# Optimization experiments

Hardware: AMD Instinct MI355X
Metric: run time of the kernel (lower is better)

Reference implementation:

```python
import jax, jax.numpy as jnp
import numpy as np

B = 512          # batch == number of memories
S = 8            # num_attention_splits
U = 512          # num_units = sum(num_units_regions)
D = 32           # dim_attention_unit
G = 8            # num_attention_groups
MASK_P = 0.1
DIM_IN = 4096
DAG = 2048       # dim_attention_global


def setup_inputs() -> dict:
    key = jax.random.key(0)
    ks = jax.random.split(key, 8)
    # xavier-normal-ish scales for the unit-wise linears
    s1 = (2.0 / (DIM_IN // S + DAG // S)) ** 0.5
    s2 = (2.0 / (DAG // S + U * D // S)) ** 0.5
    return {
        "x": jax.random.normal(ks[0], (B, DIM_IN), jnp.float32),
        "mem_attention": jax.random.normal(ks[1], (B, U, D), jnp.float32),
        "mem_outputs": jax.random.normal(ks[2], (B, U, D), jnp.float32),
        "rand_u": jax.random.uniform(ks[3], (B, B, U), jnp.float32),
        "w1": jax.random.normal(ks[4], (S, DIM_IN // S, DAG // S), jnp.float32) * s1,
        "b1": jnp.zeros((S, DAG // S), jnp.float32),
        "w2": jax.random.normal(ks[5], (S, DAG // S, U * D // S), jnp.float32) * s2,
        "b2": jnp.zeros((S, U * D // S), jnp.float32),
        "temperature": jnp.ones((U,), jnp.float32),
    }


def reference(x, mem_attention, mem_outputs, rand_u, w1, b1, w2, b2, temperature):
    # attentions(): split input, two unit-wise linears
    xs = x.reshape(B, S, DIM_IN // S)                        # [B,S,I/S]
    ga = jnp.einsum("bsi,sio->bso", xs, w1) + b1             # [B,S,DAG/S]
    att = jnp.einsum("bso,soj->bsj", ga, w2) + b2            # [B,S,U*D/S]
    att = att.reshape(B, U, D)                               # [B,U,D]
    ga_flat = ga.reshape(B, DAG)                             # [B,DAG]

    # per-unit pairwise scores: (att_b . mem_att_m) per unit  -> [B,M,U]
    weights = jnp.einsum("bud,mud->bmu", att, mem_attention)
    weights = weights * temperature                          # broadcast over U

    neg_inf = jnp.float32(-jnp.inf)
    weights = jnp.where(rand_u < MASK_P, neg_inf, weights)   # random mask
    eye = jnp.eye(B, dtype=bool)[:, :, None]                 # self-exclusion
    weights = jnp.where(eye, neg_inf, weights)

    # group-wise softmax over the memory axis
    w = weights.reshape(B, B // G, G, U)
    w = jax.nn.softmax(w, axis=1)
    w = w.reshape(B, B, U) / 8.0

    # weighted reduction over memories (avoids [B,B,U,D] intermediate)
    outputs = jnp.einsum("bmu,mud->bud", w, mem_outputs)     # [B,U,D]
    return att, ga_flat, w, outputs
```

## Files before the change

kernel.cpp:

```cpp
#include <hip/hip_runtime.h>
#include <math.h>

#define NEGBIG (-1e30f)
#define GLB_PTR(x) ((const __attribute__((address_space(1))) void*)(x))
#define LDS_PTR(x) ((__attribute__((address_space(3))) void*)(x))

typedef __bf16 bf16x8 __attribute__((ext_vector_type(8)));
typedef float  f32x4  __attribute__((ext_vector_type(4)));


__global__ __launch_bounds__(256) void gemm_split(
    const float* __restrict__ A, int lda, int Ksz,
    const float* __restrict__ Bw, int NS,
    const float* __restrict__ bias,
    float* __restrict__ C, int ldc)
{
  const int n0 = blockIdx.x * 64;
  const int b0 = blockIdx.y * 64;
  const int s  = n0 / NS;
  const float* Bp = Bw + (size_t)s * Ksz * NS;
  const int nloc0 = n0 - s * NS;
  const int acol0 = s * Ksz;

  __shared__ float As[16][64];
  __shared__ float Bs[16][64];

  const int t  = threadIdx.x;
  const int tb = t & 15, tn = t >> 4;
  float acc[4][4] = {};

  for (int k0 = 0; k0 < Ksz; k0 += 16) {
    {
      int r = t & 63, g = t >> 6;
      float4 v = *reinterpret_cast<const float4*>(
          A + (size_t)(b0 + r) * lda + acol0 + k0 + 4 * g);
      As[4*g+0][r] = v.x; As[4*g+1][r] = v.y; As[4*g+2][r] = v.z; As[4*g+3][r] = v.w;
    }
    {
      int kk = t >> 4, n4 = t & 15;
      float4 v = *reinterpret_cast<const float4*>(
          Bp + (size_t)(k0 + kk) * NS + nloc0 + 4 * n4);
      *reinterpret_cast<float4*>(&Bs[kk][4*n4]) = v;
    }
    __syncthreads();
#pragma unroll
    for (int k = 0; k < 16; ++k) {
      float4 a4 = *reinterpret_cast<const float4*>(&As[k][4*tb]);
      float4 b4 = *reinterpret_cast<const float4*>(&Bs[k][4*tn]);
      float av[4] = {a4.x, a4.y, a4.z, a4.w};
      float bv[4] = {b4.x, b4.y, b4.z, b4.w};
#pragma unroll
      for (int i = 0; i < 4; ++i)
#pragma unroll
        for (int j = 0; j < 4; ++j)
          acc[i][j] = fmaf(av[i], bv[j], acc[i][j]);
    }
    __syncthreads();
  }
#pragma unroll
  for (int i = 0; i < 4; ++i) {
    int row = b0 + 4*tb + i;
    int col = n0 + 4*tn;
    float4 o;
    o.x = acc[i][0] + bias[col + 0];
    o.y = acc[i][1] + bias[col + 1];
    o.z = acc[i][2] + bias[col + 2];
    o.w = acc[i][3] + bias[col + 3];
    *reinterpret_cast<float4*>(C + (size_t)row * ldc + col) = o;
  }
}

__global__ __launch_bounds__(256) void scores_mfma_v5(
    const float* __restrict__ att,
    const float* __restrict__ ma,
    const float* __restrict__ rnd,
    const float* __restrict__ temp,
    float* __restrict__ wout,
    float* __restrict__ stats)
{
  __shared__ float MaL[2048 * 4];
  __shared__ float tr[256 * 17];
  const int b0 = blockIdx.x * 16;
  const int u0 = blockIdx.y * 16;
  const int t  = threadIdx.x;
  const int w  = t >> 6, l = t & 63;
  const int lm = l & 15, kb = l >> 4;
  const int eu = t & 15, eb = t >> 4;
  const int gbe = b0 + eb;

  const float tmp = temp[u0 + eu];

  bf16x8 Ahi[4], Alo[4];
#pragma unroll
  for (int q = 0; q < 4; ++q) {
    const float* ap = att + (size_t)(b0 + lm) * 16384
                    + (size_t)(u0 + 4 * w + q) * 32 + kb * 8;
    float4 a0 = *reinterpret_cast<const float4*>(ap);
    float4 a1 = *reinterpret_cast<const float4*>(ap + 4);
    float af[8] = {a0.x, a0.y, a0.z, a0.w, a1.x, a1.y, a1.z, a1.w};
#pragma unroll
    for (int j = 0; j < 8; ++j) {
      __bf16 h = (__bf16)af[j];
      Ahi[q][j] = h;
      Alo[q][j] = (__bf16)(af[j] - (float)h);
    }
  }

  int off[8];
#pragma unroll
  for (int k = 0; k < 8; ++k) {
    int s = k * 256 + t;
    int mm = s >> 7, uu = (s >> 3) & 15, d4s = s & 7;
    off[k] = mm * 16384 + (u0 + uu) * 32 + ((d4s ^ (mm & 7)) << 2);
  }

  float Ls[8];
#pragma unroll
  for (int g = 0; g < 8; ++g) Ls[g] = 0.f;

  const float* rbase = rnd  + (size_t)gbe * 262144 + u0 + eu;
  float*       wbase = wout + (size_t)gbe * 262144 + u0 + eu;

#pragma unroll
  for (int k = 0; k < 8; ++k)
    __builtin_amdgcn_global_load_lds(GLB_PTR(ma + (size_t)off[k]),
                                     LDS_PTR(&MaL[(k * 256 + w * 64) * 4]), 16, 0, 0);
  float rc[16], rn[16];
#pragma unroll
  for (int j = 0; j < 16; ++j) rc[j] = rbase[(size_t)j * 512];

#pragma unroll 1
  for (int c = 0; c < 32; ++c) {
    const int m0 = c * 16;
    __syncthreads();

#pragma unroll
    for (int q = 0; q < 4; ++q) {
      const int uq = 4 * w + q;
      const int s0 = (lm << 7) + (uq << 3) + ((2 * kb)     ^ (lm & 7));
      const int s1 = (lm << 7) + (uq << 3) + ((2 * kb + 1) ^ (lm & 7));
      float4 g0 = *reinterpret_cast<const float4*>(&MaL[s0 * 4]);
      float4 g1 = *reinterpret_cast<const float4*>(&MaL[s1 * 4]);
      float bf[8] = {g0.x, g0.y, g0.z, g0.w, g1.x, g1.y, g1.z, g1.w};
      bf16x8 Bhi, Blo;
#pragma unroll
      for (int j = 0; j < 8; ++j) {
        __bf16 h = (__bf16)bf[j];
        Bhi[j] = h;
        Blo[j] = (__bf16)(bf[j] - (float)h);
      }
      f32x4 a = {0.f, 0.f, 0.f, 0.f};
      a = __builtin_amdgcn_mfma_f32_16x16x32_bf16(Ahi[q], Blo, a, 0, 0, 0);
      a = __builtin_amdgcn_mfma_f32_16x16x32_bf16(Alo[q], Bhi, a, 0, 0, 0);
      a = __builtin_amdgcn_mfma_f32_16x16x32_bf16(Ahi[q], Bhi, a, 0, 0, 0);
#pragma unroll
      for (int i = 0; i < 4; ++i) {
        const int row = (kb * 4 + i) * 16 + lm;
        tr[row * 17 + (uq ^ ((row >> 6) << 2))] = a[i];
      }
    }
    __syncthreads();

    if (c < 31) {
#pragma unroll
      for (int k = 0; k < 8; ++k)
        __builtin_amdgcn_global_load_lds(
            GLB_PTR(ma + (size_t)off[k] + (size_t)(m0 + 16) * 16384),
            LDS_PTR(&MaL[(k * 256 + w * 64) * 4]), 16, 0, 0);
#pragma unroll
      for (int j = 0; j < 16; ++j)
        rn[j] = rbase[(size_t)(m0 + 16 + j) * 512];
    }

    const int swz = (eb >> 2) << 2;
    const float* trow = &tr[(eb * 16) * 17 + (eu ^ swz)];
#pragma unroll
    for (int j = 0; j < 16; ++j) {
      const int gm = m0 + j;
      float p;
      if ((rc[j] < 0.1f) | (gm == gbe)) p = 0.f;
      else                              p = __expf(trow[j * 17] * tmp);
      wbase[(size_t)gm * 512] = p;
      Ls[j & 7] += p;
    }
#pragma unroll
    for (int j = 0; j < 16; ++j) rc[j] = rn[j];
  }

  {
    float* cell = stats + ((size_t)gbe * 512 + u0 + eu) * 32;
#pragma unroll
    for (int g = 0; g < 8; ++g) cell[g] = 1.0f / (8.0f * Ls[g]);
  }
}

__global__ __launch_bounds__(256) void emit_outputs_v4(
    const float* __restrict__ mo,
    float* __restrict__ w,
    float* __restrict__ outs)
{
  __shared__ float MoL[8 * 16 * 32];
  __shared__ float E[8 * 16 * 17];
  const int u0 = blockIdx.x * 16;
  const int b0 = blockIdx.y * 16;
  const int t  = threadIdx.x;
  const int eu = t & 15, gg = t >> 4;
  const int ma_ = gg & 7, bpar = gg >> 3;
  const int pu = t >> 4, bq = (t >> 2) & 3, dh = t & 3;

  float Sreg[8];
#pragma unroll
  for (int k = 0; k < 8; ++k)
    Sreg[k] = outs[((size_t)(b0 + bpar + 2 * k) * 512 + u0 + eu) * 32 + ma_];

  float4 acc[4][2];
#pragma unroll
  for (int i = 0; i < 4; ++i) {
    acc[i][0] = make_float4(0.f, 0.f, 0.f, 0.f);
    acc[i][1] = make_float4(0.f, 0.f, 0.f, 0.f);
  }

  float* wb = w + (size_t)(b0 + bpar) * 262144 + (size_t)ma_ * 512 + u0 + eu;

  const float* msrc0;  const float* msrc1;  const float* msrc2;  const float* msrc3;
  int loff0, loff1, loff2, loff3;
  {
    int P, mm, uu, dq;
    P = t;          mm = P >> 7; uu = (P >> 3) & 15; dq = P & 7;
    msrc0 = mo + (size_t)mm * 16384 + (size_t)(u0 + uu) * 32 + (dq ^ (uu & 7)) * 4;
    loff0 = P * 4;
    P = 256 + t;    mm = P >> 7; uu = (P >> 3) & 15; dq = P & 7;
    msrc1 = mo + (size_t)mm * 16384 + (size_t)(u0 + uu) * 32 + (dq ^ (uu & 7)) * 4;
    loff1 = P * 4;
    P = 512 + t;    mm = P >> 7; uu = (P >> 3) & 15; dq = P & 7;
    msrc2 = mo + (size_t)mm * 16384 + (size_t)(u0 + uu) * 32 + (dq ^ (uu & 7)) * 4;
    loff2 = P * 4;
    P = 768 + t;    mm = P >> 7; uu = (P >> 3) & 15; dq = P & 7;
    msrc3 = mo + (size_t)mm * 16384 + (size_t)(u0 + uu) * 32 + (dq ^ (uu & 7)) * 4;
    loff3 = P * 4;
  }

  float wpre[8];
  float4 smo0, smo1, smo2, smo3;
  {
#pragma unroll
    for (int k = 0; k < 8; ++k)
      wpre[k] = wb[(size_t)(2 * k) * 262144];
    smo0 = *reinterpret_cast<const float4*>(msrc0);
    smo1 = *reinterpret_cast<const float4*>(msrc1);
    smo2 = *reinterpret_cast<const float4*>(msrc2);
    smo3 = *reinterpret_cast<const float4*>(msrc3);
  }

#pragma unroll 1
  for (int c = 0; c < 64; ++c) {
    const int mc = c * 8;
    if (c) __syncthreads();

    {
      float* wp = wb + (size_t)mc * 512;
#pragma unroll
      for (int k = 0; k < 8; ++k) {
        float v = wpre[k] * Sreg[k];
        wp[(size_t)(2 * k) * 262144] = v;
        E[(ma_ * 16 + eu) * 17 + bpar + 2 * k] = v;
      }
    }
    *reinterpret_cast<float4*>(&MoL[loff0]) = smo0;
    *reinterpret_cast<float4*>(&MoL[loff1]) = smo1;
    *reinterpret_cast<float4*>(&MoL[loff2]) = smo2;
    *reinterpret_cast<float4*>(&MoL[loff3]) = smo3;
    __syncthreads();

    if (c < 63) {
      const float* wp = wb + (size_t)(mc + 8) * 512;
#pragma unroll
      for (int k = 0; k < 8; ++k)
        wpre[k] = wp[(size_t)(2 * k) * 262144];
      const size_t moff = (size_t)(mc + 8) * 16384;
      smo0 = *reinterpret_cast<const float4*>(msrc0 + moff);
      smo1 = *reinterpret_cast<const float4*>(msrc1 + moff);
      smo2 = *reinterpret_cast<const float4*>(msrc2 + moff);
      smo3 = *reinterpret_cast<const float4*>(msrc3 + moff);
    }

#pragma unroll
    for (int m = 0; m < 8; ++m) {
      float4 ef = *reinterpret_cast<const float4*>(&E[(m * 16 + pu) * 17 + 4 * bq]);
      float4 v0 = *reinterpret_cast<const float4*>(
          &MoL[(m * 16 + pu) * 32 + (((2 * dh) ^ (pu & 7)) * 4)]);
      float4 v1 = *reinterpret_cast<const float4*>(
          &MoL[(m * 16 + pu) * 32 + (((2 * dh + 1) ^ (pu & 7)) * 4)]);
      float es[4] = {ef.x, ef.y, ef.z, ef.w};
#pragma unroll
      for (int i = 0; i < 4; ++i) {
        acc[i][0].x = fmaf(es[i], v0.x, acc[i][0].x);
        acc[i][0].y = fmaf(es[i], v0.y, acc[i][0].y);
        acc[i][0].z = fmaf(es[i], v0.z, acc[i][0].z);
        acc[i][0].w = fmaf(es[i], v0.w, acc[i][0].w);
        acc[i][1].x = fmaf(es[i], v1.x, acc[i][1].x);
        acc[i][1].y = fmaf(es[i], v1.y, acc[i][1].y);
        acc[i][1].z = fmaf(es[i], v1.z, acc[i][1].z);
        acc[i][1].w = fmaf(es[i], v1.w, acc[i][1].w);
      }
    }
  }

#pragma unroll
  for (int i = 0; i < 4; ++i) {
    float* dst = outs + ((size_t)(b0 + 4 * bq + i) * 512 + u0 + pu) * 32 + 8 * dh;
    *reinterpret_cast<float4*>(dst)     = acc[i][0];
    *reinterpret_cast<float4*>(dst + 4) = acc[i][1];
  }
}

extern "C" void kernel_launch(void* const* d_in, const int* in_sizes, int n_in,
                              void* d_out, int out_size, void* d_ws, size_t ws_size,
                              hipStream_t stream) {
  const float* x    = (const float*)d_in[0];
  const float* ma   = (const float*)d_in[1];
  const float* mo   = (const float*)d_in[2];
  const float* rnd  = (const float*)d_in[3];
  const float* w1   = (const float*)d_in[4];
  const float* b1   = (const float*)d_in[5];
  const float* w2   = (const float*)d_in[6];
  const float* b2   = (const float*)d_in[7];
  const float* temp = (const float*)d_in[8];

  float* out  = (float*)d_out;
  float* att  = out;
  float* ga   = out + 8388608;
  float* wbuf = out + 9437184;
  float* outs = out + 143654912;

  gemm_split<<<dim3(32, 8), 256, 0, stream>>>(x, 4096, 512, w1, 256, b1, ga, 2048);
  gemm_split<<<dim3(256, 8), 256, 0, stream>>>(ga, 2048, 256, w2, 2048, b2, att, 16384);
  scores_mfma_v5<<<dim3(32, 32), 256, 0, stream>>>(att, ma, rnd, temp, wbuf, outs);
  emit_outputs_v4<<<dim3(32, 32), 256, 0, stream>>>(mo, wbuf, outs);
}
```

Measured before the change: 807.7 us.

## Fuse scores and output reduction into one two-pass kernel with recomputed scores

Merges the score kernel and the output-emission kernel into a single kernel. A first pass computes only the group-wise softmax denominators. A second pass recomputes the bf16-split MFMA scores and the mask, writes the normalized weights once, and accumulates the weighted sum over mem_outputs. It reads mem_outputs straight from global memory, using the LDS tile for the weights. This removes writing and re-reading the large unnormalized weight tensor and the intermediate stats, at the cost of reading rand_u twice and doing the MFMA work twice. It also adds a launch-bounds occupancy hint.

```diff
diff --git a/kernel.cpp b/kernel.cpp
--- a/kernel.cpp
+++ b/kernel.cpp
@@ -1,7 +1,6 @@
 #include <hip/hip_runtime.h>
 #include <math.h>
 
-#define NEGBIG (-1e30f)
 #define GLB_PTR(x) ((const __attribute__((address_space(1))) void*)(x))
 #define LDS_PTR(x) ((__attribute__((address_space(3))) void*)(x))
 
@@ -70,13 +69,45 @@
   }
 }
 
-__global__ __launch_bounds__(256) void scores_mfma_v5(
+__device__ __forceinline__ void mfma_chunk(
+    const float* MaL, float* tr,
+    const bf16x8 Ahi[4], const bf16x8 Alo[4], int w, int lm, int kb)
+{
+#pragma unroll
+  for (int q = 0; q < 4; ++q) {
+    const int uq = 4 * w + q;
+    const int s0 = (lm << 7) + (uq << 3) + ((2 * kb)     ^ (lm & 7));
+    const int s1 = (lm << 7) + (uq << 3) + ((2 * kb + 1) ^ (lm & 7));
+    float4 g0 = *reinterpret_cast<const float4*>(&MaL[s0 * 4]);
+    float4 g1 = *reinterpret_cast<const float4*>(&MaL[s1 * 4]);
+    float bf[8] = {g0.x, g0.y, g0.z, g0.w, g1.x, g1.y, g1.z, g1.w};
+    bf16x8 Bhi, Blo;
+#pragma unroll
+    for (int j = 0; j < 8; ++j) {
+      __bf16 h = (__bf16)bf[j];
+      Bhi[j] = h;
+      Blo[j] = (__bf16)(bf[j] - (float)h);
+    }
+    f32x4 a = {0.f, 0.f, 0.f, 0.f};
+    a = __builtin_amdgcn_mfma_f32_16x16x32_bf16(Ahi[q], Blo, a, 0, 0, 0);
+    a = __builtin_amdgcn_mfma_f32_16x16x32_bf16(Alo[q], Bhi, a, 0, 0, 0);
+    a = __builtin_amdgcn_mfma_f32_16x16x32_bf16(Ahi[q], Bhi, a, 0, 0, 0);
+#pragma unroll
+    for (int i = 0; i < 4; ++i) {
+      const int row = (kb * 4 + i) * 16 + lm;
+      tr[row * 17 + (uq ^ ((row >> 6) << 2))] = a[i];
+    }
+  }
+}
+
+__global__ __launch_bounds__(256, 3) void fused_back(
     const float* __restrict__ att,
     const float* __restrict__ ma,
+    const float* __restrict__ mo,
     const float* __restrict__ rnd,
     const float* __restrict__ temp,
     float* __restrict__ wout,
-    float* __restrict__ stats)
+    float* __restrict__ outs)
 {
   __shared__ float MaL[2048 * 4];
   __shared__ float tr[256 * 17];
@@ -87,6 +118,7 @@
   const int lm = l & 15, kb = l >> 4;
   const int eu = t & 15, eb = t >> 4;
   const int gbe = b0 + eb;
+  const int pu = t >> 4, bq = (t >> 2) & 3, dh = t & 3;
 
   const float tmp = temp[u0 + eu];
 
@@ -114,18 +146,21 @@
     off[k] = mm * 16384 + (u0 + uu) * 32 + ((d4s ^ (mm & 7)) << 2);
   }
 
-  float Ls[8];
-#pragma unroll
-  for (int g = 0; g < 8; ++g) Ls[g] = 0.f;
-
   const float* rbase = rnd  + (size_t)gbe * 262144 + u0 + eu;
   float*       wbase = wout + (size_t)gbe * 262144 + u0 + eu;
+  const int swz = (eb >> 2) << 2;
+  float* trow = &tr[(eb * 16) * 17 + (eu ^ swz)];
+
+  float Ls[8];
+#pragma unroll
+  for (int g = 0; g < 8; ++g) Ls[g] = 0.f;
+
+  float rc[16], rn[16];
 
 #pragma unroll
   for (int k = 0; k < 8; ++k)
     __builtin_amdgcn_global_load_lds(GLB_PTR(ma + (size_t)off[k]),
                                      LDS_PTR(&MaL[(k * 256 + w * 64) * 4]), 16, 0, 0);
-  float rc[16], rn[16];
 #pragma unroll
   for (int j = 0; j < 16; ++j) rc[j] = rbase[(size_t)j * 512];
 
@@ -133,34 +168,8 @@
   for (int c = 0; c < 32; ++c) {
     const int m0 = c * 16;
     __syncthreads();
-
-#pragma unroll
-    for (int q = 0; q < 4; ++q) {
-      const int uq = 4 * w + q;
-      const int s0 = (lm << 7) + (uq << 3) + ((2 * kb)     ^ (lm & 7));
-      const int s1 = (lm << 7) + (uq << 3) + ((2 * kb + 1) ^ (lm & 7));
-      float4 g0 = *reinterpret_cast<const float4*>(&MaL[s0 * 4]);
-      float4 g1 = *reinterpret_cast<const float4*>(&MaL[s1 * 4]);
-      float bf[8] = {g0.x, g0.y, g0.z, g0.w, g1.x, g1.y, g1.z, g1.w};
-      bf16x8 Bhi, Blo;
-#pragma unroll
-      for (int j = 0; j < 8; ++j) {
-        __bf16 h = (__bf16)bf[j];
-        Bhi[j] = h;
-        Blo[j] = (__bf16)(bf[j] - (float)h);
-      }
-      f32x4 a = {0.f, 0.f, 0.f, 0.f};
-      a = __builtin_amdgcn_mfma_f32_16x16x32_bf16(Ahi[q], Blo, a, 0, 0, 0);
-      a = __builtin_amdgcn_mfma_f32_16x16x32_bf16(Alo[q], Bhi, a, 0, 0, 0);
-      a = __builtin_amdgcn_mfma_f32_16x16x32_bf16(Ahi[q], Bhi, a, 0, 0, 0);
-#pragma unroll
-      for (int i = 0; i < 4; ++i) {
-        const int row = (kb * 4 + i) * 16 + lm;
-        tr[row * 17 + (uq ^ ((row >> 6) << 2))] = a[i];
-      }
-    }
-    __syncthreads();
-
+    mfma_chunk(MaL, tr, Ahi, Alo, w, lm, kb);
+    __syncthreads();
     if (c < 31) {
 #pragma unroll
       for (int k = 0; k < 8; ++k)
@@ -171,137 +180,78 @@
       for (int j = 0; j < 16; ++j)
         rn[j] = rbase[(size_t)(m0 + 16 + j) * 512];
     }
-
-    const int swz = (eb >> 2) << 2;
-    const float* trow = &tr[(eb * 16) * 17 + (eu ^ swz)];
+#pragma unroll
+    for (int j = 0; j < 16; ++j) {
+      const int gm = m0 + j;
+      if (!((rc[j] < 0.1f) | (gm == gbe)))
+        Ls[j & 7] += __expf(trow[j * 17] * tmp);
+    }
+#pragma unroll
+    for (int j = 0; j < 16; ++j) rc[j] = rn[j];
+  }
+
+  float IL[8];
+#pragma unroll
+  for (int g = 0; g < 8; ++g) IL[g] = 1.0f / (8.0f * Ls[g]);
+
+  float4 acc[4][2];
+#pragma unroll
+  for (int i = 0; i < 4; ++i) {
+    acc[i][0] = make_float4(0.f, 0.f, 0.f, 0.f);
+    acc[i][1] = make_float4(0.f, 0.f, 0.f, 0.f);
+  }
+#pragma unroll
+  for (int k = 0; k < 8; ++k)
+    __builtin_amdgcn_global_load_lds(GLB_PTR(ma + (size_t)off[k]),
+                                     LDS_PTR(&MaL[(k * 256 + w * 64) * 4]), 16, 0, 0);
+#pragma unroll
+  for (int j = 0; j < 16; ++j) rc[j] = rbase[(size_t)j * 512];
+
+#pragma unroll 1
+  for (int c = 0; c < 32; ++c) {
+    const int m0 = c * 16;
+    __syncthreads();
+    mfma_chunk(MaL, tr, Ahi, Alo, w, lm, kb);
+    __syncthreads();
+    if (c < 31) {
+#pragma unroll
+      for (int k = 0; k < 8; ++k)
+        __builtin_amdgcn_global_load_lds(
+            GLB_PTR(ma + (size_t)off[k] + (size_t)(m0 + 16) * 16384),
+            LDS_PTR(&MaL[(k * 256 + w * 64) * 4]), 16, 0, 0);
+#pragma unroll
+      for (int j = 0; j < 16; ++j)
+        rn[j] = rbase[(size_t)(m0 + 16 + j) * 512];
+    }
 #pragma unroll
     for (int j = 0; j < 16; ++j) {
       const int gm = m0 + j;
       float p;
       if ((rc[j] < 0.1f) | (gm == gbe)) p = 0.f;
-      else                              p = __expf(trow[j * 17] * tmp);
+      else                              p = __expf(trow[j * 17] * tmp) * IL[j & 7];
+      trow[j * 17] = p;
       wbase[(size_t)gm * 512] = p;
-      Ls[j & 7] += p;
     }
 #pragma unroll
     for (int j = 0; j < 16; ++j) rc[j] = rn[j];
-  }
-
-  {
-    float* cell = stats + ((size_t)gbe * 512 + u0 + eu) * 32;
-#pragma unroll
-    for (int g = 0; g < 8; ++g) cell[g] = 1.0f / (8.0f * Ls[g]);
-  }
-}
-
-__global__ __launch_bounds__(256) void emit_outputs_v4(
-    const float* __restrict__ mo,
-    float* __restrict__ w,
-    float* __restrict__ outs)
-{
-  __shared__ float MoL[8 * 16 * 32];
-  __shared__ float E[8 * 16 * 17];
-  const int u0 = blockIdx.x * 16;
-  const int b0 = blockIdx.y * 16;
-  const int t  = threadIdx.x;
-  const int eu = t & 15, gg = t >> 4;
-  const int ma_ = gg & 7, bpar = gg >> 3;
-  const int pu = t >> 4, bq = (t >> 2) & 3, dh = t & 3;
-
-  float Sreg[8];
-#pragma unroll
-  for (int k = 0; k < 8; ++k)
-    Sreg[k] = outs[((size_t)(b0 + bpar + 2 * k) * 512 + u0 + eu) * 32 + ma_];
-
-  float4 acc[4][2];
-#pragma unroll
-  for (int i = 0; i < 4; ++i) {
-    acc[i][0] = make_float4(0.f, 0.f, 0.f, 0.f);
-    acc[i][1] = make_float4(0.f, 0.f, 0.f, 0.f);
-  }
-
-  float* wb = w + (size_t)(b0 + bpar) * 262144 + (size_t)ma_ * 512 + u0 + eu;
-
-  const float* msrc0;  const float* msrc1;  const float* msrc2;  const float* msrc3;
-  int loff0, loff1, loff2, loff3;
-  {
-    int P, mm, uu, dq;
-    P = t;          mm = P >> 7; uu = (P >> 3) & 15; dq = P & 7;
-    msrc0 = mo + (size_t)mm * 16384 + (size_t)(u0 + uu) * 32 + (dq ^ (uu & 7)) * 4;
-    loff0 = P * 4;
-    P = 256 + t;    mm = P >> 7; uu = (P >> 3) & 15; dq = P & 7;
-    msrc1 = mo + (size_t)mm * 16384 + (size_t)(u0 + uu) * 32 + (dq ^ (uu & 7)) * 4;
-    loff1 = P * 4;
-    P = 512 + t;    mm = P >> 7; uu = (P >> 3) & 15; dq = P & 7;
-    msrc2 = mo + (size_t)mm * 16384 + (size_t)(u0 + uu) * 32 + (dq ^ (uu & 7)) * 4;
-    loff2 = P * 4;
-    P = 768 + t;    mm = P >> 7; uu = (P >> 3) & 15; dq = P & 7;
-    msrc3 = mo + (size_t)mm * 16384 + (size_t)(u0 + uu) * 32 + (dq ^ (uu & 7)) * 4;
-    loff3 = P * 4;
-  }
-
-  float wpre[8];
-  float4 smo0, smo1, smo2, smo3;
-  {
-#pragma unroll
-    for (int k = 0; k < 8; ++k)
-      wpre[k] = wb[(size_t)(2 * k) * 262144];
-    smo0 = *reinterpret_cast<const float4*>(msrc0);
-    smo1 = *reinterpret_cast<const float4*>(msrc1);
-    smo2 = *reinterpret_cast<const float4*>(msrc2);
-    smo3 = *reinterpret_cast<const float4*>(msrc3);
-  }
-
-#pragma unroll 1
-  for (int c = 0; c < 64; ++c) {
-    const int mc = c * 8;
-    if (c) __syncthreads();
-
-    {
-      float* wp = wb + (size_t)mc * 512;
-#pragma unroll
-      for (int k = 0; k < 8; ++k) {
-        float v = wpre[k] * Sreg[k];
-        wp[(size_t)(2 * k) * 262144] = v;
-        E[(ma_ * 16 + eu) * 17 + bpar + 2 * k] = v;
-      }
-    }
-    *reinterpret_cast<float4*>(&MoL[loff0]) = smo0;
-    *reinterpret_cast<float4*>(&MoL[loff1]) = smo1;
-    *reinterpret_cast<float4*>(&MoL[loff2]) = smo2;
-    *reinterpret_cast<float4*>(&MoL[loff3]) = smo3;
-    __syncthreads();
-
-    if (c < 63) {
-      const float* wp = wb + (size_t)(mc + 8) * 512;
-#pragma unroll
-      for (int k = 0; k < 8; ++k)
-        wpre[k] = wp[(size_t)(2 * k) * 262144];
-      const size_t moff = (size_t)(mc + 8) * 16384;
-      smo0 = *reinterpret_cast<const float4*>(msrc0 + moff);
-      smo1 = *reinterpret_cast<const float4*>(msrc1 + moff);
-      smo2 = *reinterpret_cast<const float4*>(msrc2 + moff);
-      smo3 = *reinterpret_cast<const float4*>(msrc3 + moff);
-    }
-
-#pragma unroll
-    for (int m = 0; m < 8; ++m) {
-      float4 ef = *reinterpret_cast<const float4*>(&E[(m * 16 + pu) * 17 + 4 * bq]);
-      float4 v0 = *reinterpret_cast<const float4*>(
-          &MoL[(m * 16 + pu) * 32 + (((2 * dh) ^ (pu & 7)) * 4)]);
-      float4 v1 = *reinterpret_cast<const float4*>(
-          &MoL[(m * 16 + pu) * 32 + (((2 * dh + 1) ^ (pu & 7)) * 4)]);
-      float es[4] = {ef.x, ef.y, ef.z, ef.w};
+    __syncthreads();
+#pragma unroll
+    for (int m = 0; m < 16; ++m) {
+      const float* mop = mo + (size_t)(m0 + m) * 16384
+                       + (size_t)(u0 + pu) * 32 + dh * 8;
+      float4 v0 = *reinterpret_cast<const float4*>(mop);
+      float4 v1 = *reinterpret_cast<const float4*>(mop + 4);
 #pragma unroll
       for (int i = 0; i < 4; ++i) {
-        acc[i][0].x = fmaf(es[i], v0.x, acc[i][0].x);
-        acc[i][0].y = fmaf(es[i], v0.y, acc[i][0].y);
-        acc[i][0].z = fmaf(es[i], v0.z, acc[i][0].z);
-        acc[i][0].w = fmaf(es[i], v0.w, acc[i][0].w);
-        acc[i][1].x = fmaf(es[i], v1.x, acc[i][1].x);
-        acc[i][1].y = fmaf(es[i], v1.y, acc[i][1].y);
-        acc[i][1].z = fmaf(es[i], v1.z, acc[i][1].z);
-        acc[i][1].w = fmaf(es[i], v1.w, acc[i][1].w);
+        float e = tr[((4 * bq + i) * 16 + m) * 17 + (pu ^ (bq << 2))];
+        acc[i][0].x = fmaf(e, v0.x, acc[i][0].x);
+        acc[i][0].y = fmaf(e, v0.y, acc[i][0].y);
+        acc[i][0].z = fmaf(e, v0.z, acc[i][0].z);
+        acc[i][0].w = fmaf(e, v0.w, acc[i][0].w);
+        acc[i][1].x = fmaf(e, v1.x, acc[i][1].x);
+        acc[i][1].y = fmaf(e, v1.y, acc[i][1].y);
+        acc[i][1].z = fmaf(e, v1.z, acc[i][1].z);
+        acc[i][1].w = fmaf(e, v1.w, acc[i][1].w);
       }
     }
   }
@@ -335,6 +285,5 @@
 
   gemm_split<<<dim3(32, 8), 256, 0, stream>>>(x, 4096, 512, w1, 256, b1, ga, 2048);
   gemm_split<<<dim3(256, 8), 256, 0, stream>>>(ga, 2048, 256, w2, 2048, b2, att, 16384);
-  scores_mfma_v5<<<dim3(32, 32), 256, 0, stream>>>(att, ma, rnd, temp, wbuf, outs);
-  emit_outputs_v4<<<dim3(32, 32), 256, 0, stream>>>(mo, wbuf, outs);
-}
+  fused_back<<<dim3(32, 32), 256, 0, stream>>>(att, ma, mo, rnd, temp, wbuf, outs);
+}
```

Result: slower. 1.690 ms (+109.3%).

## Retile emit_outputs to 8 batch rows per block with remapped block order

Applied to the files above, without the earlier changes.

The output-emission kernel now handles 8 batch rows by 16 units per block instead of 16x16, launching a 1D grid of 2048 blocks with a swizzled block-to-tile mapping. Each thread loads and stores the softmax weights as a float4 over 4 consecutive units rather than scalar strided accesses, and accumulates a 4x4 output tile. This aims at more coalesced weight read/modify/write traffic and more blocks for occupancy, at the cost of re-reading mem_outputs from global twice as often.

```diff
diff --git a/kernel.cpp b/kernel.cpp
--- a/kernel.cpp
+++ b/kernel.cpp
@@ -1,7 +1,6 @@
 #include <hip/hip_runtime.h>
 #include <math.h>
 
-#define NEGBIG (-1e30f)
 #define GLB_PTR(x) ((const __attribute__((address_space(1))) void*)(x))
 #define LDS_PTR(x) ((__attribute__((address_space(3))) void*)(x))
 
@@ -194,33 +193,31 @@
   }
 }
 
-__global__ __launch_bounds__(256) void emit_outputs_v4(
+__global__ __launch_bounds__(256) void emit_outputs_v5(
     const float* __restrict__ mo,
     float* __restrict__ w,
     float* __restrict__ outs)
 {
   __shared__ float MoL[8 * 16 * 32];
-  __shared__ float E[8 * 16 * 17];
-  const int u0 = blockIdx.x * 16;
-  const int b0 = blockIdx.y * 16;
-  const int t  = threadIdx.x;
-  const int eu = t & 15, gg = t >> 4;
-  const int ma_ = gg & 7, bpar = gg >> 3;
-  const int pu = t >> 4, bq = (t >> 2) & 3, dh = t & 3;
-
-  float Sreg[8];
-#pragma unroll
-  for (int k = 0; k < 8; ++k)
-    Sreg[k] = outs[((size_t)(b0 + bpar + 2 * k) * 512 + u0 + eu) * 32 + ma_];
-
-  float4 acc[4][2];
-#pragma unroll
-  for (int i = 0; i < 4; ++i) {
-    acc[i][0] = make_float4(0.f, 0.f, 0.f, 0.f);
-    acc[i][1] = make_float4(0.f, 0.f, 0.f, 0.f);
-  }
-
-  float* wb = w + (size_t)(b0 + bpar) * 262144 + (size_t)ma_ * 512 + u0 + eu;
+  __shared__ float E[8 * 16 * 12];
+  const int bid = blockIdx.x;
+  const int id  = (bid & 7) * 256 + (bid >> 3);
+  const int b0  = (id & 63) * 8;
+  const int u0  = (id >> 6) * 16;
+  const int t   = threadIdx.x;
+  const int uq = t & 3, am = (t >> 2) & 7, bh = t >> 5;
+  const int pu = t >> 4, bh2 = (t >> 3) & 1, dh = t & 7;
+
+  float Sreg[4];
+#pragma unroll
+  for (int e = 0; e < 4; ++e)
+    Sreg[e] = outs[((size_t)(b0 + bh) * 512 + u0 + 4 * uq + e) * 32 + am];
+
+  float4 acc[4];
+#pragma unroll
+  for (int i = 0; i < 4; ++i) acc[i] = make_float4(0.f, 0.f, 0.f, 0.f);
+
+  float* wb = w + (size_t)(b0 + bh) * 262144 + (size_t)am * 512 + u0 + 4 * uq;
 
   const float* msrc0;  const float* msrc1;  const float* msrc2;  const float* msrc3;
   int loff0, loff1, loff2, loff3;
@@ -240,17 +237,12 @@
     loff3 = P * 4;
   }
 
-  float wpre[8];
-  float4 smo0, smo1, smo2, smo3;
-  {
-#pragma unroll
-    for (int k = 0; k < 8; ++k)
-      wpre[k] = wb[(size_t)(2 * k) * 262144];
-    smo0 = *reinterpret_cast<const float4*>(msrc0);
-    smo1 = *reinterpret_cast<const float4*>(msrc1);
-    smo2 = *reinterpret_cast<const float4*>(msrc2);
-    smo3 = *reinterpret_cast<const float4*>(msrc3);
-  }
+  float4 wpre, smo0, smo1, smo2, smo3;
+  wpre = *reinterpret_cast<const float4*>(wb);
+  smo0 = *reinterpret_cast<const float4*>(msrc0);
+  smo1 = *reinterpret_cast<const float4*>(msrc1);
+  smo2 = *reinterpret_cast<const float4*>(msrc2);
+  smo3 = *reinterpret_cast<const float4*>(msrc3);
 
 #pragma unroll 1
   for (int c = 0; c < 64; ++c) {
@@ -258,13 +250,16 @@
     if (c) __syncthreads();
 
     {
-      float* wp = wb + (size_t)mc * 512;
-#pragma unroll
-      for (int k = 0; k < 8; ++k) {
-        float v = wpre[k] * Sreg[k];
-        wp[(size_t)(2 * k) * 262144] = v;
-        E[(ma_ * 16 + eu) * 17 + bpar + 2 * k] = v;
-      }
+      float4 vv;
+      vv.x = wpre.x * Sreg[0];
+      vv.y = wpre.y * Sreg[1];
+      vv.z = wpre.z * Sreg[2];
+      vv.w = wpre.w * Sreg[3];
+      *reinterpret_cast<float4*>(wb + (size_t)mc * 512) = vv;
+      E[(am * 16 + 4 * uq + 0) * 12 + bh] = vv.x;
+      E[(am * 16 + 4 * uq + 1) * 12 + bh] = vv.y;
+      E[(am * 16 + 4 * uq + 2) * 12 + bh] = vv.z;
+      E[(am * 16 + 4 * uq + 3) * 12 + bh] = vv.w;
     }
     *reinterpret_cast<float4*>(&MoL[loff0]) = smo0;
     *reinterpret_cast<float4*>(&MoL[loff1]) = smo1;
@@ -273,10 +268,7 @@
     __syncthreads();
 
     if (c < 63) {
-      const float* wp = wb + (size_t)(mc + 8) * 512;
-#pragma unroll
-      for (int k = 0; k < 8; ++k)
-        wpre[k] = wp[(size_t)(2 * k) * 262144];
+      wpre = *reinterpret_cast<const float4*>(wb + (size_t)(mc + 8) * 512);
       const size_t moff = (size_t)(mc + 8) * 16384;
       smo0 = *reinterpret_cast<const float4*>(msrc0 + moff);
       smo1 = *reinterpret_cast<const float4*>(msrc1 + moff);
@@ -286,31 +278,32 @@
 
 #pragma unroll
     for (int m = 0; m < 8; ++m) {
-      float4 ef = *reinterpret_cast<const float4*>(&E[(m * 16 + pu) * 17 + 4 * bq]);
-      float4 v0 = *reinterpret_cast<const float4*>(
-          &MoL[(m * 16 + pu) * 32 + (((2 * dh) ^ (pu & 7)) * 4)]);
-      float4 v1 = *reinterpret_cast<const float4*>(
-          &MoL[(m * 16 + pu) * 32 + (((2 * dh + 1) ^ (pu & 7)) * 4)]);
-      float es[4] = {ef.x, ef.y, ef.z, ef.w};
-#pragma unroll
-      for (int i = 0; i < 4; ++i) {
-        acc[i][0].x = fmaf(es[i], v0.x, acc[i][0].x);
-        acc[i][0].y = fmaf(es[i], v0.y, acc[i][0].y);
-        acc[i][0].z = fmaf(es[i], v0.z, acc[i][0].z);
-        acc[i][0].w = fmaf(es[i], v0.w, acc[i][0].w);
-        acc[i][1].x = fmaf(es[i], v1.x, acc[i][1].x);
-        acc[i][1].y = fmaf(es[i], v1.y, acc[i][1].y);
-        acc[i][1].z = fmaf(es[i], v1.z, acc[i][1].z);
-        acc[i][1].w = fmaf(es[i], v1.w, acc[i][1].w);
-      }
+      float4 ef = *reinterpret_cast<const float4*>(&E[(m * 16 + pu) * 12 + 4 * bh2]);
+      float4 v  = *reinterpret_cast<const float4*>(
+          &MoL[(m * 16 + pu) * 32 + ((dh ^ (pu & 7)) * 4)]);
+      acc[0].x = fmaf(ef.x, v.x, acc[0].x);
+      acc[0].y = fmaf(ef.x, v.y, acc[0].y);
+      acc[0].z = fmaf(ef.x, v.z, acc[0].z);
+      acc[0].w = fmaf(ef.x, v.w, acc[0].w);
+      acc[1].x = fmaf(ef.y, v.x, acc[1].x);
+      acc[1].y = fmaf(ef.y, v.y, acc[1].y);
+      acc[1].z = fmaf(ef.y, v.z, acc[1].z);
+      acc[1].w = fmaf(ef.y, v.w, acc[1].w);
+      acc[2].x = fmaf(ef.z, v.x, acc[2].x);
+      acc[2].y = fmaf(ef.z, v.y, acc[2].y);
+      acc[2].z = fmaf(ef.z, v.z, acc[2].z);
+      acc[2].w = fmaf(ef.z, v.w, acc[2].w);
+      acc[3].x = fmaf(ef.w, v.x, acc[3].x);
+      acc[3].y = fmaf(ef.w, v.y, acc[3].y);
+      acc[3].z = fmaf(ef.w, v.z, acc[3].z);
+      acc[3].w = fmaf(ef.w, v.w, acc[3].w);
     }
   }
 
 #pragma unroll
   for (int i = 0; i < 4; ++i) {
-    float* dst = outs + ((size_t)(b0 + 4 * bq + i) * 512 + u0 + pu) * 32 + 8 * dh;
-    *reinterpret_cast<float4*>(dst)     = acc[i][0];
-    *reinterpret_cast<float4*>(dst + 4) = acc[i][1];
+    float* dst = outs + ((size_t)(b0 + 4 * bh2 + i) * 512 + u0 + pu) * 32 + dh * 4;
+    *reinterpret_cast<float4*>(dst) = acc[i];
   }
 }
 
@@ -336,5 +329,5 @@
   gemm_split<<<dim3(32, 8), 256, 0, stream>>>(x, 4096, 512, w1, 256, b1, ga, 2048);
   gemm_split<<<dim3(256, 8), 256, 0, stream>>>(ga, 2048, 256, w2, 2048, b2, att, 16384);
   scores_mfma_v5<<<dim3(32, 32), 256, 0, stream>>>(att, ma, rnd, temp, wbuf, outs);
-  emit_outputs_v4<<<dim3(32, 32), 256, 0, stream>>>(mo, wbuf, outs);
+  emit_outputs_v5<<<dim3(2048), 256, 0, stream>>>(mo, wbuf, outs);
 }
```

New measurement: 859.9 us. +6.5%, slower.
